# Kernel optimization log

Measured on AMD Instinct MI355X. Metric: run time of the kernel, lower is better.

## Reference

```python
import jax, jax.numpy as jnp
import numpy as np

B, S, H = 1, 2048, 4096
NH, NKV, HD = 32, 8, 128  # 32 query heads, 8 kv heads (GQA), head_dim 128
THETA = 10000.0


def setup_inputs() -> dict:
    key = jax.random.key(0)
    k0, k1, k2, k3, k4 = jax.random.split(key, 5)
    sc = 0.02
    hidden_states = jax.random.normal(k0, (B, S, H), jnp.float32)
    wq = jax.random.normal(k1, (H, NH * HD), jnp.float32) * sc
    wk = jax.random.normal(k2, (H, NKV * HD), jnp.float32) * sc
    wv = jax.random.normal(k3, (H, NKV * HD), jnp.float32) * sc
    wo = jax.random.normal(k4, (NH * HD, H), jnp.float32) * sc
    # precompute_freqs_cis(head_dim, S): angles[t, i] = t / theta^(2i/d)
    freqs = 1.0 / (THETA ** (jnp.arange(0, HD, 2, dtype=jnp.float32) / HD))  # [HD/2]
    ang = jnp.outer(jnp.arange(S, dtype=jnp.float32), freqs)  # [S, HD/2]
    return {"hidden_states": hidden_states, "wq": wq, "wk": wk, "wv": wv,
            "wo": wo, "cos": jnp.cos(ang), "sin": jnp.sin(ang)}


def _rope(x, cos, sin):
    # x: [B,S,h,HD]; pairs (x[...,2i], x[...,2i+1]) form complex numbers,
    # multiplied by freqs_cis = cos + i*sin (broadcast over heads).
    xr = x[..., 0::2]
    xi = x[..., 1::2]
    c = cos[None, :, None, :]
    s = sin[None, :, None, :]
    out_r = xr * c - xi * s
    out_i = xr * s + xi * c
    return jnp.stack([out_r, out_i], axis=-1).reshape(x.shape)


def reference(hidden_states, wq, wk, wv, wo, cos, sin):
    b, s, _ = hidden_states.shape
    q = (hidden_states @ wq).reshape(b, s, NH, HD)
    k = (hidden_states @ wk).reshape(b, s, NKV, HD)
    v = (hidden_states @ wv).reshape(b, s, NKV, HD)
    q = _rope(q, cos, sin)
    k = _rope(k, cos, sin)
    # repeat_kv: interleaved repeat of kv heads to match query heads (GQA)
    n_rep = NH // NKV
    k = jnp.repeat(k, n_rep, axis=2)  # [b,s,NH,HD]
    v = jnp.repeat(v, n_rep, axis=2)
    scale = 1.0 / np.sqrt(HD).astype(np.float32)
    scores = jnp.einsum('bqhd,bkhd->bhqk', q, k) * scale  # [b,NH,s,s]
    causal = jnp.tril(jnp.ones((s, s), dtype=bool))
    scores = jnp.where(causal[None, None], scores, jnp.finfo(scores.dtype).min)
    probs = jax.nn.softmax(scores, axis=-1)
    attn = jnp.einsum('bhqk,bkhd->bqhd', probs, v).reshape(b, s, NH * HD)
    return attn @ wo
```

## Files before the change

kernel.cpp:

```cpp
#include <hip/hip_runtime.h>

typedef __bf16 bf16x8 __attribute__((ext_vector_type(8)));
typedef float f32x4 __attribute__((ext_vector_type(4)));

__device__ __forceinline__ unsigned short f2bf(float f) {
    unsigned u = __builtin_bit_cast(unsigned, f);
    u += 0x7FFFu + ((u >> 16) & 1u);
    return (unsigned short)(u >> 16);
}

__device__ __forceinline__ void gload16(void* lds, const void* g) {
    __builtin_amdgcn_global_load_lds((const __attribute__((address_space(1))) void*)g,
                                     (__attribute__((address_space(3))) void*)lds,
                                     16, 0, 0);
}

__global__ void k_cvt(const float* __restrict__ in, unsigned short* __restrict__ out, int n8) {
    int i = blockIdx.x * blockDim.x + threadIdx.x;
    if (i >= n8) return;
    float4 a = ((const float4*)in)[i * 2];
    float4 b = ((const float4*)in)[i * 2 + 1];
    ushort4 r0 = { f2bf(a.x), f2bf(a.y), f2bf(a.z), f2bf(a.w) };
    ushort4 r1 = { f2bf(b.x), f2bf(b.y), f2bf(b.z), f2bf(b.w) };
    ((ushort4*)out)[i * 2]     = r0;
    ((ushort4*)out)[i * 2 + 1] = r1;
}

__global__ void k_transpose(const float* __restrict__ in, unsigned short* __restrict__ out,
                            int K, int N) {
    __shared__ float tile[32][33];
    int n0 = blockIdx.x * 32, k0 = blockIdx.y * 32;
    int tx = threadIdx.x, ty = threadIdx.y;
#pragma unroll
    for (int i = 0; i < 32; i += 8)
        tile[ty + i][tx] = in[(size_t)(k0 + ty + i) * N + n0 + tx];
    __syncthreads();
#pragma unroll
    for (int i = 0; i < 32; i += 8)
        out[(size_t)(n0 + ty + i) * K + k0 + tx] = f2bf(tile[tx][ty + i]);
}

template <int MODE>
__global__ __launch_bounds__(256) void k_gemm(
    const unsigned short* __restrict__ A,
    const unsigned short* __restrict__ Bt,
    int N,
    unsigned short* __restrict__ qkvo,
    unsigned short* __restrict__ vto,
    const float* __restrict__ cosT,
    const float* __restrict__ sinT,
    float* __restrict__ fout)
{
    __shared__ unsigned short As[128 * 32];
    __shared__ unsigned short Bs[128 * 32];
    const int K = 4096;
    int tid = threadIdx.x, wid = tid >> 6, lane = tid & 63;
    int lr = lane & 15, lg = lane >> 4;
    int m0 = blockIdx.y * 128, n0 = blockIdx.x * 128;
    int wm = (wid >> 1) * 64, wn = (wid & 1) * 64;

    f32x4 acc[4][4] = {};

    int ca = wid * 64 + lane;
    int am = ca >> 2;
    int ak = (ca & 3) * 8;
    const unsigned short* Ap1 = A  + (size_t)(m0 + am)      * K + ak;
    const unsigned short* Ap2 = A  + (size_t)(m0 + am + 64) * K + ak;
    const unsigned short* Bp1 = Bt + (size_t)(n0 + am)      * K + ak;
    const unsigned short* Bp2 = Bt + (size_t)(n0 + am + 64) * K + ak;
    unsigned short* Ad1 = &As[(wid * 64) * 8];
    unsigned short* Ad2 = &As[(256 + wid * 64) * 8];
    unsigned short* Bd1 = &Bs[(wid * 64) * 8];
    unsigned short* Bd2 = &Bs[(256 + wid * 64) * 8];

    for (int k0 = 0; k0 < K; k0 += 32) {
        gload16(Ad1, Ap1 + k0);
        gload16(Ad2, Ap2 + k0);
        gload16(Bd1, Bp1 + k0);
        gload16(Bd2, Bp2 + k0);
        __syncthreads();
        bf16x8 af[4], bfr[4];
#pragma unroll
        for (int i = 0; i < 4; i++)
            af[i] = *(const bf16x8*)&As[(wm + i * 16 + lr) * 32 + lg * 8];
#pragma unroll
        for (int i = 0; i < 4; i++)
            bfr[i] = *(const bf16x8*)&Bs[(wn + i * 16 + lr) * 32 + lg * 8];
#pragma unroll
        for (int i = 0; i < 4; i++)
#pragma unroll
            for (int j = 0; j < 4; j++)
                acc[i][j] = __builtin_amdgcn_mfma_f32_16x16x32_bf16(af[i], bfr[j], acc[i][j], 0, 0, 0);
        __syncthreads();
    }

    if (MODE == 0) {
#pragma unroll
        for (int j = 0; j < 4; j++) {
            int ng = n0 + wn + j * 16 + lr;
            int d = ng & 127;
            bool isv = (ng >= 5120);
#pragma unroll
            for (int i = 0; i < 4; i++) {
#pragma unroll
                for (int r = 0; r < 4; r++) {
                    int sg = m0 + wm + i * 16 + lg * 4 + r;
                    float v = acc[i][j][r];
                    float part = __shfl_xor(v, 1, 64);
                    if (!isv) {
                        float cc = cosT[sg * 64 + (d >> 1)];
                        float ss = sinT[sg * 64 + (d >> 1)];
                        v = (d & 1) ? fmaf(part, ss, v * cc) : fmaf(-part, ss, v * cc);
                        qkvo[(size_t)sg * 6144 + ng] = f2bf(v);
                    } else {
                        vto[(size_t)(ng - 5120) * 2048 + sg] = f2bf(v);
                    }
                }
            }
        }
    } else {
#pragma unroll
        for (int j = 0; j < 4; j++) {
            int ng = n0 + wn + j * 16 + lr;
#pragma unroll
            for (int i = 0; i < 4; i++) {
#pragma unroll
                for (int r = 0; r < 4; r++) {
                    int sg = m0 + wm + i * 16 + lg * 4 + r;
                    fout[(size_t)sg * 4096 + ng] = acc[i][j][r];
                }
            }
        }
    }
}

__global__ __launch_bounds__(256) void k_attn(
    const unsigned short* __restrict__ qkv,
    const unsigned short* __restrict__ vt,
    unsigned short* __restrict__ ao)
{
    __shared__ unsigned short Ks[32 * 128];
    __shared__ unsigned short Vs[128 * 32];
    __shared__ unsigned short Ps[4 * 16 * 32];

    int tid = threadIdx.x, w = tid >> 6, lane = tid & 63;
    int lr = lane & 15, lg = lane >> 4;
    int h = blockIdx.x & 31;
    int qt = 31 - (blockIdx.x >> 5);
    int q0 = qt * 64, kvh = h >> 2;

    int qrow = q0 + w * 16 + lr;
    const unsigned short* qp = qkv + (size_t)qrow * 6144 + h * 128 + lg * 8;
    bf16x8 aq[4];
#pragma unroll
    for (int kb = 0; kb < 4; kb++) aq[kb] = *(const bf16x8*)(qp + kb * 32);

    f32x4 o[8] = {};
    float m[4], l[4];
#pragma unroll
    for (int r = 0; r < 4; r++) { m[r] = -1e30f; l[r] = 0.f; }
    constexpr float SCL2 = 0.08838834764831845f * 1.44269504088896340f;

    int c1 = w * 64 + lane;
    int kp1 = c1 >> 4, pc1 = c1 & 15;
    const unsigned short* kgp = qkv + (size_t)kp1 * 6144 + 4096 + kvh * 128 + (pc1 ^ (kp1 & 7)) * 8;
    int d1 = c1 >> 2, pcv = c1 & 3;
    const unsigned short* vgp = vt + (size_t)(kvh * 128 + d1) * 2048 + (pcv ^ (d1 & 3)) * 8;
    unsigned short* Kd1 = &Ks[(w * 64) * 8];
    unsigned short* Kd2 = &Ks[(256 + w * 64) * 8];
    unsigned short* Vd1 = &Vs[(w * 64) * 8];
    unsigned short* Vd2 = &Vs[(256 + w * 64) * 8];

    int nt = 2 * (qt + 1);
    for (int t = 0; t < nt; ++t) {
        int kp0 = t * 32;
        gload16(Kd1, kgp + (size_t)kp0 * 6144);
        gload16(Kd2, kgp + (size_t)kp0 * 6144 + (size_t)16 * 6144);
        gload16(Vd1, vgp + kp0);
        gload16(Vd2, vgp + kp0 + 64 * 2048);
        __syncthreads();

        if (kp0 <= q0 + w * 16 + 15) {
            f32x4 sc[2] = {};
#pragma unroll
            for (int cb = 0; cb < 2; ++cb) {
                int kp = cb * 16 + lr;
#pragma unroll
                for (int kb = 0; kb < 4; ++kb) {
                    int dcl = kb * 4 + lg;
                    bf16x8 bk = *(const bf16x8*)&Ks[kp * 128 + ((dcl ^ (kp & 7)) * 8)];
                    sc[cb] = __builtin_amdgcn_mfma_f32_16x16x32_bf16(aq[kb], bk, sc[cb], 0, 0, 0);
                }
            }
            if (kp0 + 31 > q0 + w * 16) {
#pragma unroll
                for (int cb = 0; cb < 2; ++cb) {
                    int kpg = kp0 + cb * 16 + lr;
#pragma unroll
                    for (int r = 0; r < 4; r++) {
                        int qg = q0 + w * 16 + lg * 4 + r;
                        if (kpg > qg) sc[cb][r] = -1e30f;
                    }
                }
            }
            float tm[4];
#pragma unroll
            for (int r = 0; r < 4; r++) tm[r] = fmaxf(sc[0][r], sc[1][r]);
#pragma unroll
            for (int off = 1; off < 16; off <<= 1)
#pragma unroll
                for (int r = 0; r < 4; r++) tm[r] = fmaxf(tm[r], __shfl_xor(tm[r], off, 64));
            float al[4], rs[4];
#pragma unroll
            for (int r = 0; r < 4; r++) {
                float mn = fmaxf(m[r], tm[r]);
                al[r] = exp2f((m[r] - mn) * SCL2);
                m[r] = mn;
                rs[r] = 0.f;
            }
#pragma unroll
            for (int cb = 0; cb < 2; cb++)
#pragma unroll
                for (int r = 0; r < 4; r++) {
                    float p = exp2f((sc[cb][r] - m[r]) * SCL2);
                    sc[cb][r] = p;
                    rs[r] += p;
                }
#pragma unroll
            for (int off = 1; off < 16; off <<= 1)
#pragma unroll
                for (int r = 0; r < 4; r++) rs[r] += __shfl_xor(rs[r], off, 64);
#pragma unroll
            for (int r = 0; r < 4; r++) l[r] = l[r] * al[r] + rs[r];
#pragma unroll
            for (int db = 0; db < 8; db++)
#pragma unroll
                for (int r = 0; r < 4; r++) o[db][r] *= al[r];
#pragma unroll
            for (int cb = 0; cb < 2; cb++)
#pragma unroll
                for (int r = 0; r < 4; r++) {
                    int q = lg * 4 + r, kp = cb * 16 + lr;
                    Ps[w * 512 + q * 32 + (((kp >> 3) ^ (q & 3)) * 8) + (kp & 7)] = f2bf(sc[cb][r]);
                }
            asm volatile("s_waitcnt lgkmcnt(0)" ::: "memory");
            bf16x8 pa = *(const bf16x8*)&Ps[w * 512 + lr * 32 + ((lg ^ (lr & 3)) * 8)];
#pragma unroll
            for (int db = 0; db < 8; db++) {
                int d = db * 16 + lr;
                bf16x8 bv = *(const bf16x8*)&Vs[d * 32 + ((lg ^ (d & 3)) * 8)];
                o[db] = __builtin_amdgcn_mfma_f32_16x16x32_bf16(pa, bv, o[db], 0, 0, 0);
            }
        }
        __syncthreads();
    }

#pragma unroll
    for (int r = 0; r < 4; r++) l[r] = 1.0f / l[r];
#pragma unroll
    for (int db = 0; db < 8; db++)
#pragma unroll
        for (int r = 0; r < 4; r++) {
            int qg = q0 + w * 16 + lg * 4 + r;
            ao[(size_t)qg * 4096 + h * 128 + db * 16 + lr] = f2bf(o[db][r] * l[r]);
        }
}

extern "C" void kernel_launch(void* const* d_in, const int* in_sizes, int n_in,
                              void* d_out, int out_size, void* d_ws, size_t ws_size,
                              hipStream_t stream) {
    const float* hs   = (const float*)d_in[0];
    const float* wq   = (const float*)d_in[1];
    const float* wk   = (const float*)d_in[2];
    const float* wv   = (const float*)d_in[3];
    const float* wo   = (const float*)d_in[4];
    const float* cosT = (const float*)d_in[5];
    const float* sinT = (const float*)d_in[6];
    float* out = (float*)d_out;

    unsigned short* hsb   = (unsigned short*)d_ws;
    unsigned short* wqkvT = hsb   + (size_t)2048 * 4096;
    unsigned short* woT   = wqkvT + (size_t)6144 * 4096;
    unsigned short* qkvb  = woT   + (size_t)4096 * 4096;
    unsigned short* vtb   = qkvb  + (size_t)2048 * 6144;
    unsigned short* attnb = vtb   + (size_t)1024 * 2048;

    k_cvt<<<4096, 256, 0, stream>>>(hs, hsb, 1048576);
    dim3 tb(32, 8);
    k_transpose<<<dim3(128, 128), tb, 0, stream>>>(wq, wqkvT, 4096, 4096);
    k_transpose<<<dim3(32, 128),  tb, 0, stream>>>(wk, wqkvT + (size_t)4096 * 4096, 4096, 1024);
    k_transpose<<<dim3(32, 128),  tb, 0, stream>>>(wv, wqkvT + (size_t)5120 * 4096, 4096, 1024);
    k_transpose<<<dim3(128, 128), tb, 0, stream>>>(wo, woT, 4096, 4096);

    k_gemm<0><<<dim3(48, 16), 256, 0, stream>>>(hsb, wqkvT, 6144, qkvb, vtb, cosT, sinT, nullptr);
    k_attn<<<1024, 256, 0, stream>>>(qkvb, vtb, attnb);
    k_gemm<1><<<dim3(32, 16), 256, 0, stream>>>(attnb, woT, 4096, nullptr, nullptr, nullptr, nullptr, out);
}
```

Baseline: 567.1 us.

## Rewrite GEMMs as 8-wave 256-row tiles with double-buffered swizzled LDS pipeline

Replaces the simple 128x128 single-buffered GEMM with an 8-wave kernel using 256xBN tiles, K-step 64, double-buffered LDS fed by direct global-to-LDS loads, XOR-swizzled LDS layout to avoid bank conflicts, and a workgroup-id swizzle for L2 locality. MFMA phases are interleaved with LDS reads and next-tile prefetch, using barriers and s_setprio to overlap memory with compute. It targets the sync-bound, poorly overlapped main loop of the QKV and output projections. The hand-placed waitcnts make correctness depend on the exact load counts, and the LDS footprint is large.

```diff
diff --git a/kernel.cpp b/kernel.cpp
--- a/kernel.cpp
+++ b/kernel.cpp
@@ -40,71 +40,128 @@
         out[(size_t)(n0 + ty + i) * K + k0 + tx] = f2bf(tile[tx][ty + i]);
 }
 
-template <int MODE>
-__global__ __launch_bounds__(256) void k_gemm(
+#define MFMA_HALF(MH)                                                                   \
+    _Pragma("unroll") for (int ii = 0; ii < 4; ++ii)                                    \
+        _Pragma("unroll") for (int j = 0; j < NREP; ++j)                                \
+            acc[(MH) * 4 + ii][j] = __builtin_amdgcn_mfma_f32_16x16x32_bf16(            \
+                a[ii], b[j], acc[(MH) * 4 + ii][j], 0, 0, 0);
+
+template <int BN, int MODE>
+__global__ __launch_bounds__(512, 2) void k_gemm8(
     const unsigned short* __restrict__ A,
     const unsigned short* __restrict__ Bt,
-    int N,
+    int GX,
     unsigned short* __restrict__ qkvo,
     unsigned short* __restrict__ vto,
     const float* __restrict__ cosT,
     const float* __restrict__ sinT,
     float* __restrict__ fout)
 {
-    __shared__ unsigned short As[128 * 32];
-    __shared__ unsigned short Bs[128 * 32];
-    const int K = 4096;
-    int tid = threadIdx.x, wid = tid >> 6, lane = tid & 63;
-    int lr = lane & 15, lg = lane >> 4;
-    int m0 = blockIdx.y * 128, n0 = blockIdx.x * 128;
-    int wm = (wid >> 1) * 64, wn = (wid & 1) * 64;
-
-    f32x4 acc[4][4] = {};
-
-    int ca = wid * 64 + lane;
-    int am = ca >> 2;
-    int ak = (ca & 3) * 8;
-    const unsigned short* Ap1 = A  + (size_t)(m0 + am)      * K + ak;
-    const unsigned short* Ap2 = A  + (size_t)(m0 + am + 64) * K + ak;
-    const unsigned short* Bp1 = Bt + (size_t)(n0 + am)      * K + ak;
-    const unsigned short* Bp2 = Bt + (size_t)(n0 + am + 64) * K + ak;
-    unsigned short* Ad1 = &As[(wid * 64) * 8];
-    unsigned short* Ad2 = &As[(256 + wid * 64) * 8];
-    unsigned short* Bd1 = &Bs[(wid * 64) * 8];
-    unsigned short* Bd2 = &Bs[(256 + wid * 64) * 8];
-
-    for (int k0 = 0; k0 < K; k0 += 32) {
-        gload16(Ad1, Ap1 + k0);
-        gload16(Ad2, Ap2 + k0);
-        gload16(Bd1, Bp1 + k0);
-        gload16(Bd2, Bp2 + k0);
-        __syncthreads();
-        bf16x8 af[4], bfr[4];
-#pragma unroll
-        for (int i = 0; i < 4; i++)
-            af[i] = *(const bf16x8*)&As[(wm + i * 16 + lr) * 32 + lg * 8];
-#pragma unroll
-        for (int i = 0; i < 4; i++)
-            bfr[i] = *(const bf16x8*)&Bs[(wn + i * 16 + lr) * 32 + lg * 8];
-#pragma unroll
-        for (int i = 0; i < 4; i++)
-#pragma unroll
-            for (int j = 0; j < 4; j++)
-                acc[i][j] = __builtin_amdgcn_mfma_f32_16x16x32_bf16(af[i], bfr[j], acc[i][j], 0, 0, 0);
-        __syncthreads();
-    }
-
-    if (MODE == 0) {
-#pragma unroll
-        for (int j = 0; j < 4; j++) {
-            int ng = n0 + wn + j * 16 + lr;
-            int d = ng & 127;
-            bool isv = (ng >= 5120);
-#pragma unroll
-            for (int i = 0; i < 4; i++) {
-#pragma unroll
-                for (int r = 0; r < 4; r++) {
-                    int sg = m0 + wm + i * 16 + lg * 4 + r;
+    constexpr int K = 4096, NT = 64;
+    constexpr int NREP = BN / 64;
+    constexpr int AL = 4, BL = BN / 64;
+    __shared__ unsigned short As[2][256 * 64];
+    __shared__ unsigned short Bs[2][BN * 64];
+
+    const int tid = threadIdx.x;
+    const int wid = tid >> 6, lane = tid & 63;
+    const int lr = lane & 15, lg = lane >> 4;
+    const int wr = wid >> 2, wc = wid & 3;
+
+    const int nwg = gridDim.x;
+    const int id = blockIdx.x;
+    const int swzid = (id & 7) * (nwg >> 3) + (id >> 3);
+    const int bx = swzid % GX, by = swzid / GX;
+    const int m0 = by * 256, n0 = bx * BN;
+
+    f32x4 acc[8][NREP] = {};
+
+    auto stageA = [&](int ts, int bsel) {
+#pragma unroll
+        for (int l = 0; l < AL; ++l) {
+            int c = l * 512 + tid;
+            int row = c >> 3, ch = c & 7;
+            gload16(&As[bsel][c * 8],
+                    A + (size_t)(m0 + row) * K + ts * 64 + ((ch ^ (row & 7)) * 8));
+        }
+    };
+    auto stageB = [&](int ts, int bsel) {
+#pragma unroll
+        for (int l = 0; l < BL; ++l) {
+            int c = l * 512 + tid;
+            int row = c >> 3, ch = c & 7;
+            gload16(&Bs[bsel][c * 8],
+                    Bt + (size_t)(n0 + row) * K + ts * 64 + ((ch ^ (row & 7)) * 8));
+        }
+    };
+    auto readA = [&](int bsel, int mh, int kh, bf16x8* a) {
+#pragma unroll
+        for (int ii = 0; ii < 4; ++ii) {
+            int row = wr * 128 + (mh * 4 + ii) * 16 + lr;
+            a[ii] = *(const bf16x8*)&As[bsel][row * 64 + ((((kh << 2) | lg) ^ (row & 7)) * 8)];
+        }
+    };
+    auto readB = [&](int bsel, int kh, bf16x8* b) {
+#pragma unroll
+        for (int j = 0; j < NREP; ++j) {
+            int row = wc * (BN / 4) + j * 16 + lr;
+            b[j] = *(const bf16x8*)&Bs[bsel][row * 64 + ((((kh << 2) | lg) ^ (row & 7)) * 8)];
+        }
+    };
+
+    auto ktile = [&](int t, int cb) {
+        bf16x8 a[4], b[NREP];
+        readA(cb, 0, 0, a); readB(cb, 0, b);
+        stageA((t + 1) & (NT - 1), cb ^ 1);
+        __builtin_amdgcn_s_barrier();
+        asm volatile("s_waitcnt lgkmcnt(0)" ::: "memory");
+        __builtin_amdgcn_s_setprio(1);
+        MFMA_HALF(0)
+        __builtin_amdgcn_s_setprio(0);
+        __builtin_amdgcn_s_barrier();
+        readA(cb, 1, 0, a);
+        __builtin_amdgcn_s_barrier();
+        asm volatile("s_waitcnt lgkmcnt(0)" ::: "memory");
+        __builtin_amdgcn_s_setprio(1);
+        MFMA_HALF(1)
+        __builtin_amdgcn_s_setprio(0);
+        __builtin_amdgcn_s_barrier();
+        readA(cb, 0, 1, a); readB(cb, 1, b);
+        __builtin_amdgcn_s_barrier();
+        asm volatile("s_waitcnt lgkmcnt(0)" ::: "memory");
+        __builtin_amdgcn_s_setprio(1);
+        MFMA_HALF(0)
+        __builtin_amdgcn_s_setprio(0);
+        __builtin_amdgcn_s_barrier();
+        readA(cb, 1, 1, a);
+        stageB((t + 2) & (NT - 1), cb);
+        __builtin_amdgcn_s_barrier();
+        asm volatile("s_waitcnt lgkmcnt(0)" ::: "memory");
+        __builtin_amdgcn_s_setprio(1);
+        MFMA_HALF(1)
+        __builtin_amdgcn_s_setprio(0);
+        asm volatile("s_waitcnt vmcnt(%0)" :: "n"(BL) : "memory");
+        __builtin_amdgcn_s_barrier();
+    };
+
+    stageA(0, 0); stageB(0, 0); stageB(1, 1);
+    asm volatile("s_waitcnt vmcnt(%0)" :: "n"(BL) : "memory");
+    __builtin_amdgcn_s_barrier();
+
+    for (int tt = 0; tt < NT / 2; ++tt) { ktile(2 * tt, 0); ktile(2 * tt + 1, 1); }
+    asm volatile("s_waitcnt vmcnt(0)" ::: "memory");
+
+    if constexpr (MODE == 0) {
+#pragma unroll
+        for (int j = 0; j < NREP; ++j) {
+            const int ng = n0 + wc * (BN / 4) + j * 16 + lr;
+            const int d = ng & 127;
+            const bool isv = (ng >= 5120);
+#pragma unroll
+            for (int i = 0; i < 8; ++i) {
+#pragma unroll
+                for (int r = 0; r < 4; ++r) {
+                    const int sg = m0 + wr * 128 + i * 16 + lg * 4 + r;
                     float v = acc[i][j][r];
                     float part = __shfl_xor(v, 1, 64);
                     if (!isv) {
@@ -120,13 +177,13 @@
         }
     } else {
 #pragma unroll
-        for (int j = 0; j < 4; j++) {
-            int ng = n0 + wn + j * 16 + lr;
-#pragma unroll
-            for (int i = 0; i < 4; i++) {
-#pragma unroll
-                for (int r = 0; r < 4; r++) {
-                    int sg = m0 + wm + i * 16 + lg * 4 + r;
+        for (int j = 0; j < NREP; ++j) {
+            const int ng = n0 + wc * (BN / 4) + j * 16 + lr;
+#pragma unroll
+            for (int i = 0; i < 8; ++i) {
+#pragma unroll
+                for (int r = 0; r < 4; ++r) {
+                    const int sg = m0 + wr * 128 + i * 16 + lg * 4 + r;
                     fout[(size_t)sg * 4096 + ng] = acc[i][j][r];
                 }
             }
@@ -292,7 +349,7 @@
     k_transpose<<<dim3(32, 128),  tb, 0, stream>>>(wv, wqkvT + (size_t)5120 * 4096, 4096, 1024);
     k_transpose<<<dim3(128, 128), tb, 0, stream>>>(wo, woT, 4096, 4096);
 
-    k_gemm<0><<<dim3(48, 16), 256, 0, stream>>>(hsb, wqkvT, 6144, qkvb, vtb, cosT, sinT, nullptr);
+    k_gemm8<256, 0><<<192, 512, 0, stream>>>(hsb, wqkvT, 24, qkvb, vtb, cosT, sinT, nullptr);
     k_attn<<<1024, 256, 0, stream>>>(qkvb, vtb, attnb);
-    k_gemm<1><<<dim3(32, 16), 256, 0, stream>>>(attnb, woT, 4096, nullptr, nullptr, nullptr, nullptr, out);
-}
+    k_gemm8<128, 1><<<256, 512, 0, stream>>>(attnb, woT, 32, nullptr, nullptr, nullptr, nullptr, out);
+}
```

Measured after the change: 586.3 us. +3.4%, slower.
